# Performance work log

Hardware: AMD Instinct MI355X
Metric: run time of the kernel (lower is better)

Reference implementation:

```python
import jax, jax.numpy as jnp
import numpy as np

H = 512


def setup_inputs() -> dict:
    key = jax.random.key(0)
    ks = jax.random.split(key, 20)
    B, S, T, V, WD = 128, 80, 28, 8000, 1024
    sc = 0.02
    return {
        "encoder_hidden_state": jax.random.normal(ks[0], (1, B, H), jnp.float32),
        "encoder_outputs": jax.random.normal(ks[1], (B, S, H), jnp.float32),
        "target_sentences": jax.random.randint(ks[2], (B, T), 0, V),
        "training_steps": -200,
        "emb": jax.random.normal(ks[3], (V, WD), jnp.float32) * sc,
        "fc1_w": jax.random.normal(ks[4], (H, 2 * H), jnp.float32) * sc,
        "fc1_b": jnp.zeros((H,), jnp.float32),
        "fc2_w": jax.random.normal(ks[5], (H, H), jnp.float32) * sc,
        "fc2_b": jnp.zeros((H,), jnp.float32),
        "fc3_w": jax.random.normal(ks[6], (H, H), jnp.float32) * sc,
        "fc3_b": jnp.zeros((H,), jnp.float32),
        "fc4_w": jax.random.normal(ks[7], (H, H), jnp.float32) * sc,
        "fc4_b": jnp.zeros((H,), jnp.float32),
        "attn_w": jax.random.normal(ks[8], (H,), jnp.float32) * sc,
        "w_ih": jax.random.normal(ks[9], (4 * H, H + WD), jnp.float32) * sc,
        "w_hh": jax.random.normal(ks[10], (4 * H, H), jnp.float32) * sc,
        "b_ih": jnp.zeros((4 * H,), jnp.float32),
        "b_hh": jnp.zeros((4 * H,), jnp.float32),
        "out_w": jax.random.normal(ks[11], (V, H), jnp.float32) * sc,
        "out_b": jnp.zeros((V,), jnp.float32),
    }


def reference(encoder_hidden_state, encoder_outputs, target_sentences, training_steps,
              emb, fc1_w, fc1_b, fc2_w, fc2_b, fc3_w, fc3_b, fc4_w, fc4_b,
              attn_w, w_ih, w_hh, b_ih, b_hh, out_w, out_b):
    # With training_steps=-200, teacher-forcing threshold expit(-9.15)~1e-4, so
    # random.uniform(0.05,0.995) > threshold always holds -> target embedding used every step.
    tgt_emb = emb[target_sentences]              # (B, T, WD)
    xs = jnp.swapaxes(tgt_emb[:, :-1], 0, 1)     # (T-1, B, WD)
    h0 = encoder_hidden_state[0]                 # (B, H)
    c0 = jnp.zeros_like(h0)

    def step(carry, x_t):
        h, c = carry
        # additive-style attention: 4 stacked Linear layers (no nonlinearity, as in source)
        hs = jnp.broadcast_to(h[:, None, :], encoder_outputs.shape)
        z = jnp.concatenate([encoder_outputs, hs], axis=-1)      # (B, S, 2H)
        a = z @ fc1_w.T + fc1_b
        a = a @ fc2_w.T + fc2_b
        a = a @ fc3_w.T + fc3_b
        a = a @ fc4_w.T + fc4_b
        scores = a @ attn_w                                       # (B, S)
        wts = jax.nn.softmax(scores, axis=1)
        ctx = jnp.einsum('bs,bsd->bd', wts, encoder_outputs)      # (B, H)
        # single LSTM step (torch gate order i, f, g, o)
        li = jnp.concatenate([x_t, ctx], axis=1)                  # (B, WD+H)
        gates = li @ w_ih.T + b_ih + h @ w_hh.T + b_hh
        i_, f_, g_, o_ = jnp.split(gates, 4, axis=1)
        c_new = jax.nn.sigmoid(f_) * c + jax.nn.sigmoid(i_) * jnp.tanh(g_)
        h_new = jax.nn.sigmoid(o_) * jnp.tanh(c_new)
        logits = h_new @ out_w.T + out_b                          # (B, V)
        return (h_new, c_new), logits

    _, logits = jax.lax.scan(step, (h0, c0), xs)                  # (T-1, B, V)
    logits = jnp.swapaxes(logits, 0, 1)                           # (B, T-1, V)
    preds = jnp.argmax(logits, axis=2)
    return logits, preds
```

## Files before the change

kernel.cpp:

```cpp
#include <hip/hip_runtime.h>
#include <math.h>

#define BB 128
#define SS 80
#define HH 512
#define TT 27
#define TFULL 28
#define VV 8000

typedef __attribute__((ext_vector_type(4))) float f32x4;
typedef __attribute__((ext_vector_type(8))) short bfrag;

#define OFF_VA   0
#define OFF_VB   512
#define OFF_U    1024
#define OFF_PART 1536
#define OFF_CTX  17920
#define OFF_GB   83456
#define OFF_XG   345600
#define OFF_BAR  7423488
#define FP32_WS_FLOATS 7489536
#define O_H3     0
#define O_WHI    3670016
#define O_WLO    4718592
#define O_R      5767168
#define O_A3X    O_R
#define O_B3X    (O_R + 10616832)
#define O_B3L    O_R

__device__ __forceinline__ unsigned short f2bf(float x) {
    unsigned int u = __float_as_uint(x);
    unsigned int r = (u + 0x7fff + ((u >> 16) & 1)) >> 16;
    return (unsigned short)r;
}
__device__ __forceinline__ float bf2f(unsigned short h) {
    return __uint_as_float(((unsigned int)h) << 16);
}
__device__ __forceinline__ void gload16(void* lds, const void* g) {
    __builtin_amdgcn_global_load_lds(
        (__attribute__((address_space(1))) void*)g,
        (__attribute__((address_space(3))) void*)lds, 16, 0, 0);
}
__device__ __forceinline__ void gload16s(void* lds, const void* g) {
    __builtin_amdgcn_global_load_lds(
        (__attribute__((address_space(1))) void*)g,
        (__attribute__((address_space(3))) void*)lds, 16, 0, 1);
}

__global__ __launch_bounds__(256) void zero_bar(unsigned* b) {
    int i = blockIdx.x * 256 + threadIdx.x;
    if (i < 16512) b[i] = 0u;
}

__global__ __launch_bounds__(256) void conv_split(
    const float* __restrict__ src, int ld, int koff, int K,
    int mode, int bside, const int* __restrict__ gidx,
    unsigned short* __restrict__ dst)
{
    int r = blockIdx.x;
    int sr = r;
    if (mode == 1) { int b = r & 127, t = r >> 7; sr = gidx[b * TFULL + t]; }
    const float* s = src + (size_t)sr * ld + koff;
    unsigned short* d = dst + (size_t)r * (3 * K);
    int off_mid = bside ? 2 * K : K;
    int off_lo  = bside ? K : 2 * K;
    for (int c = threadIdx.x * 4; c < K; c += 1024) {
        float4 v = *(const float4*)(s + c);
        ushort4 hi, lo;
        hi.x = f2bf(v.x); lo.x = f2bf(v.x - bf2f(hi.x));
        hi.y = f2bf(v.y); lo.y = f2bf(v.y - bf2f(hi.y));
        hi.z = f2bf(v.z); lo.z = f2bf(v.z - bf2f(hi.z));
        hi.w = f2bf(v.w); lo.w = f2bf(v.w - bf2f(hi.w));
        *(ushort4*)(d + c) = hi;
        *(ushort4*)(d + off_mid + c) = hi;
        *(ushort4*)(d + off_lo + c) = lo;
    }
}

__global__ __launch_bounds__(256) void conv_splitc(
    const float* __restrict__ src, unsigned short* __restrict__ dst)
{
    int r = blockIdx.x;
    const float* s = src + (size_t)r * 512;
    unsigned short* d = dst + (size_t)r * 1024;
    int c = threadIdx.x * 2;
    float2 v = *(const float2*)(s + c);
    unsigned short hx = f2bf(v.x), hy = f2bf(v.y);
    d[c] = hx; d[c + 1] = hy;
    d[512 + c] = f2bf(v.x - bf2f(hx));
    d[512 + c + 1] = f2bf(v.y - bf2f(hy));
}

__global__ __launch_bounds__(256) void conv_splitw(
    const float* __restrict__ src,
    unsigned short* __restrict__ whi, unsigned short* __restrict__ wlo)
{
    int r = blockIdx.x;
    int sr = (r & 3) * 512 + (r >> 2);
    const float* s = src + (size_t)sr * 512;
    int c = threadIdx.x * 2;
    float2 v = *(const float2*)(s + c);
    unsigned short hx = f2bf(v.x), hy = f2bf(v.y);
    whi[(size_t)r * 512 + c] = hx;
    whi[(size_t)r * 512 + c + 1] = hy;
    wlo[(size_t)r * 512 + c] = f2bf(v.x - bf2f(hx));
    wlo[(size_t)r * 512 + c + 1] = f2bf(v.y - bf2f(hy));
}

__global__ __launch_bounds__(256) void gemm_bf16_nt(
    int M, int N, int K3,
    const unsigned short* __restrict__ A3, int astride, int ahalf,
    const unsigned short* __restrict__ B3,
    const float* __restrict__ bias,
    const float* __restrict__ addmat,
    float* __restrict__ C, int outMode)
{
    __shared__ unsigned short Asm[128 * 64];
    __shared__ unsigned short Bsm[128 * 64];
    int tid = threadIdx.x, wave = tid >> 6, lane = tid & 63;

    int nT = gridDim.x, mT = gridDim.y;
    int p = blockIdx.y * nT + blockIdx.x;
    int nwg = nT * mT;
    int q = nwg >> 3, rr = nwg & 7;
    int xcd = p & 7, pos = p >> 3;
    int lid = (xcd < rr) ? (xcd * (q + 1) + pos) : (rr * (q + 1) + (xcd - rr) * q + pos);
    const int GROUP = 9;
    int width = GROUP * nT;
    int gid2 = lid / width;
    int first_m = gid2 * GROUP;
    int gsz = mT - first_m; if (gsz > GROUP) gsz = GROUP;
    int rem = lid - gid2 * width;
    int mt = first_m + rem % gsz;
    int nt = rem / gsz;
    int m0 = mt * 128, n0 = nt * 128;

    int wm0 = (wave >> 1) * 64, wn0 = (wave & 1) * 64;
    f32x4 acc[4][4];
    #pragma unroll
    for (int i = 0; i < 4; ++i)
        #pragma unroll
        for (int j = 0; j < 4; ++j) acc[i][j] = (f32x4){0.f, 0.f, 0.f, 0.f};

    int srow8 = lane >> 3;
    int schunk = lane & 7;
    for (int k0 = 0; k0 < K3; k0 += 64) {
        int ek0 = ahalf ? (k0 >= 512 ? k0 - 512 : k0) : k0;
        #pragma unroll
        for (int rep = 0; rep < 4; ++rep) {
            int ci = wave * 4 + rep;
            int row = ci * 8 + srow8;
            int sc = schunk ^ (row & 7);
            int gm = m0 + row; if (gm >= M) gm = M - 1;
            gload16(Asm + ci * 512 + lane * 8,
                    A3 + (size_t)gm * astride + ek0 + sc * 8);
            int gn = n0 + row; if (gn >= N) gn = N - 1;
            gload16(Bsm + ci * 512 + lane * 8,
                    B3 + (size_t)gn * K3 + k0 + sc * 8);
        }
        __syncthreads();
        #pragma unroll
        for (int ks = 0; ks < 2; ++ks) {
            bfrag a[4], b[4];
            #pragma unroll
            for (int i = 0; i < 4; ++i) {
                int ar = wm0 + i * 16 + (lane & 15);
                int ab = (ar * 128 + ks * 64 + (lane >> 4) * 16) ^ ((ar & 7) << 4);
                a[i] = *(const bfrag*)((const char*)Asm + ab);
                int br = wn0 + i * 16 + (lane & 15);
                int bb = (br * 128 + ks * 64 + (lane >> 4) * 16) ^ ((br & 7) << 4);
                b[i] = *(const bfrag*)((const char*)Bsm + bb);
            }
            #pragma unroll
            for (int i = 0; i < 4; ++i)
                #pragma unroll
                for (int j = 0; j < 4; ++j)
                    acc[i][j] = __builtin_amdgcn_mfma_f32_16x16x32_bf16(a[i], b[j], acc[i][j], 0, 0, 0);
        }
        __syncthreads();
    }
    #pragma unroll
    for (int i = 0; i < 4; ++i) {
        #pragma unroll
        for (int r = 0; r < 4; ++r) {
            int m = m0 + wm0 + i * 16 + ((lane >> 4) << 2) + r;
            if (m >= M) continue;
            #pragma unroll
            for (int j = 0; j < 4; ++j) {
                int n = n0 + wn0 + j * 16 + (lane & 15);
                if (n >= N) continue;
                float v = acc[i][j][r];
                if (bias) v += bias[n];
                if (addmat) v += addmat[(size_t)(m & 127) * 2048 + n];
                size_t oi;
                if (outMode == 0) oi = (size_t)m * N + n;
                else { int bb2 = m & 127, tt = m >> 7; oi = ((size_t)bb2 * TT + tt) * (size_t)VV + n; }
                C[oi] = v;
            }
        }
    }
}

__global__ __launch_bounds__(256, 1) void lstm_persist4(
    unsigned short* __restrict__ H3,
    const unsigned short* __restrict__ Whi,
    const unsigned short* __restrict__ Wlo,
    const float* __restrict__ xgb,
    unsigned* bar)
{
    __shared__ unsigned short Wl[64 * 512];
    __shared__ unsigned short Al[16 * 1024];
    __shared__ int s_ids[2];

    int tid = threadIdx.x, wv = tid >> 6, lane = tid & 63;
    if (tid == 0) {
        unsigned x;
        asm volatile("s_getreg_b32 %0, hwreg(HW_REG_XCC_ID)" : "=s"(x));
        x &= 7u;
        unsigned s = __hip_atomic_fetch_add(bar + 16384 + x * 16, 1u,
                        __ATOMIC_RELAXED, __HIP_MEMORY_SCOPE_AGENT);
        s_ids[0] = (int)x;
        s_ids[1] = (int)(s & 31u);
    }
    __syncthreads();
    int xcd = s_ids[0], slot = s_ids[1];
    int b0 = xcd * 16;
    int nq0 = slot * 64;

    int l15 = lane & 15, g4 = (lane >> 4) << 4;
    int arow = l15;
    int wr = wv * 16 + l15;
    int n_local = wv * 16 + l15;
    int g = n_local & 3;
    int kglob = slot * 16 + (n_local >> 2);
    const unsigned short* wloRow = Wlo + (size_t)(nq0 + n_local) * 512;
    float creg[4] = {0.f, 0.f, 0.f, 0.f};

    {
        const unsigned short* Wsrc = Whi + (size_t)nq0 * 512;
        #pragma unroll
        for (int j = 0; j < 16; ++j) {
            int ci = j * 256 + tid;
            int row = ci >> 6, cc = ci & 63;
            int sc = cc ^ (row & 7);
            gload16(Wl + ci * 8, Wsrc + (size_t)row * 512 + sc * 8);
        }
        asm volatile("s_waitcnt vmcnt(0)" ::: "memory");
    }
    __syncthreads();

    for (int t = 0; t < TT; ++t) {
        const unsigned short* Asrc = H3 + ((size_t)t * 128 + b0) * 1024;
        #pragma unroll
        for (int j = 0; j < 8; ++j) {
            int ci = j * 256 + tid;
            int row = ci >> 7, cc = ci & 127;
            int sc = cc ^ (row & 7);
            gload16s(Al + ci * 8, Asrc + (size_t)row * 1024 + sc * 8);
        }
        asm volatile("s_waitcnt vmcnt(0)" ::: "memory");
        __syncthreads();

        f32x4 acc0 = (f32x4){0.f, 0.f, 0.f, 0.f};
        f32x4 acc1 = acc0;
        #pragma unroll
        for (int c = 0; c < 16; ++c) {
            int ab = (arow * 2048 + c * 64 + g4) ^ ((arow & 7) << 4);
            int wb = (wr * 1024 + c * 64 + g4) ^ ((wr & 7) << 4);
            bfrag a = *(const bfrag*)((const char*)Al + ab);
            bfrag w = *(const bfrag*)((const char*)Wl + wb);
            if (c & 1) acc1 = __builtin_amdgcn_mfma_f32_16x16x32_bf16(a, w, acc1, 0, 0, 0);
            else       acc0 = __builtin_amdgcn_mfma_f32_16x16x32_bf16(a, w, acc0, 0, 0, 0);
        }
        #pragma unroll
        for (int c = 0; c < 16; ++c) {
            int ab = (arow * 2048 + c * 64 + g4) ^ ((arow & 7) << 4);
            bfrag a = *(const bfrag*)((const char*)Al + ab);
            bfrag w = *(const bfrag*)(wloRow + c * 32 + (lane >> 4) * 8);
            if (c & 1) acc1 = __builtin_amdgcn_mfma_f32_16x16x32_bf16(a, w, acc1, 0, 0, 0);
            else       acc0 = __builtin_amdgcn_mfma_f32_16x16x32_bf16(a, w, acc0, 0, 0, 0);
        }
        #pragma unroll
        for (int c = 0; c < 16; ++c) {
            int ab = (arow * 2048 + (16 + c) * 64 + g4) ^ ((arow & 7) << 4);
            int wb = (wr * 1024 + c * 64 + g4) ^ ((wr & 7) << 4);
            bfrag a = *(const bfrag*)((const char*)Al + ab);
            bfrag w = *(const bfrag*)((const char*)Wl + wb);
            if (c & 1) acc1 = __builtin_amdgcn_mfma_f32_16x16x32_bf16(a, w, acc1, 0, 0, 0);
            else       acc0 = __builtin_amdgcn_mfma_f32_16x16x32_bf16(a, w, acc0, 0, 0, 0);
        }
        f32x4 accT = acc0 + acc1;

        #pragma unroll
        for (int r = 0; r < 4; ++r) {
            int m_local = ((lane >> 4) << 2) + r;
            int b = b0 + m_local;
            float v = accT[r] +
                      xgb[(((size_t)t * 128 + b) << 11) + (size_t)g * 512 + kglob];
            float f1 = __shfl_down(v, 1);
            float f2 = __shfl_down(v, 2);
            float f3 = __shfl_down(v, 3);
            if ((lane & 3) == 0) {
                float si = 1.f / (1.f + expf(-v));
                float sf = 1.f / (1.f + expf(-f1));
                float tg = tanhf(f2);
                float so = 1.f / (1.f + expf(-f3));
                float cn = sf * creg[r] + si * tg;
                float hn = so * tanhf(cn);
                creg[r] = cn;
                unsigned short hi = f2bf(hn);
                unsigned short lo = f2bf(hn - bf2f(hi));
                unsigned short* hr = H3 + ((size_t)(t + 1) * 128 + b) * 1024;
                hr[kglob] = hi; hr[512 + kglob] = lo;
            }
        }

        if (t != TT - 1) {
            asm volatile("s_waitcnt vmcnt(0)" ::: "memory");
            __syncthreads();
            unsigned ph = (unsigned)(t + 1);
            if (tid == 0)
                __hip_atomic_store(bar + xcd * 2048 + slot * 16, ph,
                                   __ATOMIC_RELAXED, __HIP_MEMORY_SCOPE_AGENT);
            if (tid < 32) {
                unsigned* fl = bar + xcd * 2048 + tid * 16;
                while (__hip_atomic_load(fl, __ATOMIC_RELAXED,
                                         __HIP_MEMORY_SCOPE_AGENT) < ph)
                    __builtin_amdgcn_s_sleep(1);
            }
            __syncthreads();
        }
    }
}

__global__ __launch_bounds__(512) void matvec_col_partial(
    const float* __restrict__ W, int ldw, int koff,
    const float* __restrict__ vin, float* __restrict__ part)
{
    int k = threadIdx.x;
    int o0 = blockIdx.x * 16;
    float acc = 0.f;
    #pragma unroll
    for (int o = 0; o < 16; ++o)
        acc += W[(size_t)(o0 + o) * ldw + koff + k] * vin[o0 + o];
    part[blockIdx.x * 512 + k] = acc;
}

__global__ __launch_bounds__(512) void matvec_combine(
    const float* __restrict__ part, float* __restrict__ vout)
{
    int k = threadIdx.x;
    float s = 0.f;
    #pragma unroll
    for (int c = 0; c < 32; ++c) s += part[c * 512 + k];
    vout[k] = s;
}

__global__ __launch_bounds__(256) void attn_ctx(
    const float* __restrict__ enc, const float* __restrict__ u,
    float* __restrict__ ctx)
{
    __shared__ float su[HH];
    __shared__ float sw[SS];
    __shared__ float ssum;
    int b = blockIdx.x, tid = threadIdx.x;
    su[tid] = u[tid];
    su[tid + 256] = u[tid + 256];
    __syncthreads();
    const float* eb = enc + (size_t)b * SS * HH;
    int wave = tid >> 6, lane = tid & 63;
    for (int s = wave; s < SS; s += 4) {
        const float* row = eb + s * HH;
        float acc = 0.f;
        for (int k = lane; k < HH; k += 64) acc += row[k] * su[k];
        #pragma unroll
        for (int off = 32; off; off >>= 1) acc += __shfl_down(acc, off);
        if (lane == 0) sw[s] = acc;
    }
    __syncthreads();
    if (tid == 0) {
        float mx = sw[0];
        for (int s = 1; s < SS; ++s) mx = fmaxf(mx, sw[s]);
        float sum = 0.f;
        for (int s = 0; s < SS; ++s) { float e = expf(sw[s] - mx); sw[s] = e; sum += e; }
        ssum = sum;
    }
    __syncthreads();
    float inv = 1.0f / ssum;
    for (int k = tid; k < HH; k += 256) {
        float acc = 0.f;
        #pragma unroll 4
        for (int s = 0; s < SS; ++s) acc += sw[s] * eb[s * HH + k];
        ctx[(size_t)b * HH + k] = acc * inv;
    }
}

__global__ __launch_bounds__(256) void gemm_nt(
    int M, int N, int K,
    const float* __restrict__ A, int lda,
    const float* __restrict__ Bm, int ldb, int kob,
    const float* __restrict__ bias1, const float* __restrict__ bias2,
    float* __restrict__ C)
{
    __shared__ float As[16][132];
    __shared__ float Bs[16][132];
    int tid = threadIdx.x;
    int m0 = blockIdx.y * 128, n0 = blockIdx.x * 128;
    int tn = tid & 15, tm = tid >> 4;
    float acc[8][8];
    #pragma unroll
    for (int i = 0; i < 8; ++i)
        #pragma unroll
        for (int j = 0; j < 8; ++j) acc[i][j] = 0.f;
    int lr = tid >> 2;
    int lk = (tid & 3) * 4;
    for (int k0 = 0; k0 < K; k0 += 16) {
        #pragma unroll
        for (int half = 0; half < 2; ++half) {
            int mr = lr + half * 64;
            int m = m0 + mr;
            float4 va = make_float4(0.f, 0.f, 0.f, 0.f);
            if (m < M) va = *(const float4*)(A + (size_t)m * lda + k0 + lk);
            As[lk + 0][mr] = va.x; As[lk + 1][mr] = va.y;
            As[lk + 2][mr] = va.z; As[lk + 3][mr] = va.w;
            int n = n0 + mr;
            float4 vb = make_float4(0.f, 0.f, 0.f, 0.f);
            if (n < N) vb = *(const float4*)(Bm + (size_t)n * ldb + kob + k0 + lk);
            Bs[lk + 0][mr] = vb.x; Bs[lk + 1][mr] = vb.y;
            Bs[lk + 2][mr] = vb.z; Bs[lk + 3][mr] = vb.w;
        }
        __syncthreads();
        #pragma unroll
        for (int kk = 0; kk < 16; ++kk) {
            float4 a0 = *(const float4*)&As[kk][tm * 8];
            float4 a1 = *(const float4*)&As[kk][tm * 8 + 4];
            float4 b0 = *(const float4*)&Bs[kk][tn * 8];
            float4 b1 = *(const float4*)&Bs[kk][tn * 8 + 4];
            float av[8] = {a0.x, a0.y, a0.z, a0.w, a1.x, a1.y, a1.z, a1.w};
            float bv[8] = {b0.x, b0.y, b0.z, b0.w, b1.x, b1.y, b1.z, b1.w};
            #pragma unroll
            for (int i = 0; i < 8; ++i)
                #pragma unroll
                for (int j = 0; j < 8; ++j)
                    acc[i][j] += av[i] * bv[j];
        }
        __syncthreads();
    }
    #pragma unroll
    for (int i = 0; i < 8; ++i) {
        int m = m0 + tm * 8 + i;
        if (m >= M) continue;
        #pragma unroll
        for (int j = 0; j < 8; ++j) {
            int n = n0 + tn * 8 + j;
            if (n >= N) continue;
            float v = acc[i][j];
            if (bias1) v += bias1[n];
            if (bias2) v += bias2[n];
            C[(size_t)m * N + n] = v;
        }
    }
}

__global__ __launch_bounds__(256) void argmax_k(
    const float* __restrict__ logits, float* __restrict__ preds)
{
    int r = blockIdx.x * 4 + (threadIdx.x >> 6);
    int lane = threadIdx.x & 63;
    const float* row = logits + (size_t)r * VV;
    float best = -INFINITY;
    int bi = 0;
    for (int v = lane; v < VV; v += 64) {
        float x = row[v];
        if (x > best) { best = x; bi = v; }
    }
    #pragma unroll
    for (int off = 32; off; off >>= 1) {
        float ob = __shfl_down(best, off);
        int oi = __shfl_down(bi, off);
        if (ob > best || (ob == best && oi < bi)) { best = ob; bi = oi; }
    }
    if (lane == 0) preds[r] = (float)bi;
}

extern "C" void kernel_launch(void* const* d_in, const int* in_sizes, int n_in,
                              void* d_out, int out_size, void* d_ws, size_t ws_size,
                              hipStream_t stream) {
    const float* ehs   = (const float*)d_in[0];
    const float* enc   = (const float*)d_in[1];
    const int*   tgt   = (const int*)d_in[2];
    const float* emb   = (const float*)d_in[4];
    const float* fc1w  = (const float*)d_in[5];
    const float* fc2w  = (const float*)d_in[7];
    const float* fc3w  = (const float*)d_in[9];
    const float* fc4w  = (const float*)d_in[11];
    const float* attnw = (const float*)d_in[13];
    const float* wih   = (const float*)d_in[14];
    const float* whh   = (const float*)d_in[15];
    const float* bih   = (const float*)d_in[16];
    const float* bhh   = (const float*)d_in[17];
    const float* outw  = (const float*)d_in[18];
    const float* outb  = (const float*)d_in[19];
    float* out = (float*)d_out;
    float* ws  = (float*)d_ws;

    float* vA   = ws + OFF_VA;
    float* vB   = ws + OFF_VB;
    float* u    = ws + OFF_U;
    float* part = ws + OFF_PART;
    float* ctx  = ws + OFF_CTX;
    float* gb   = ws + OFF_GB;
    float* xg   = ws + OFF_XG;
    unsigned* bar = (unsigned*)(ws + OFF_BAR);
    unsigned short* bfb = (unsigned short*)(ws + FP32_WS_FLOATS);
    unsigned short* H3   = bfb + O_H3;
    unsigned short* WHI  = bfb + O_WHI;
    unsigned short* WLO  = bfb + O_WLO;
    unsigned short* A3X  = bfb + O_A3X;
    unsigned short* B3X  = bfb + O_B3X;
    unsigned short* B3L  = bfb + O_B3L;

    matvec_col_partial<<<32, 512, 0, stream>>>(fc4w, 512, 0, attnw, part);
    matvec_combine<<<1, 512, 0, stream>>>(part, vA);
    matvec_col_partial<<<32, 512, 0, stream>>>(fc3w, 512, 0, vA, part);
    matvec_combine<<<1, 512, 0, stream>>>(part, vB);
    matvec_col_partial<<<32, 512, 0, stream>>>(fc2w, 512, 0, vB, part);
    matvec_combine<<<1, 512, 0, stream>>>(part, vA);
    matvec_col_partial<<<32, 512, 0, stream>>>(fc1w, 1024, 0, vA, part);
    matvec_combine<<<1, 512, 0, stream>>>(part, u);

    attn_ctx<<<128, 256, 0, stream>>>(enc, u, ctx);

    {
        dim3 g(16, 1);
        gemm_nt<<<g, 256, 0, stream>>>(128, 2048, 512, ctx, 512,
                                       wih, 1536, 1024, bih, bhh, gb);
    }

    conv_split<<<2048, 256, 0, stream>>>(wih, 1536, 0, 1024, 0, 1, nullptr, B3X);
    conv_split<<<3456, 256, 0, stream>>>(emb, 1024, 0, 1024, 1, 0, tgt, A3X);
    {
        dim3 g(16, 27);
        gemm_bf16_nt<<<g, 256, 0, stream>>>(3456, 2048, 3072, A3X, 3072, 0, B3X,
                                            nullptr, gb, xg, 0);
    }

    conv_split<<<8000, 256, 0, stream>>>(outw, 512, 0, 512, 0, 1, nullptr, B3L);
    conv_splitw<<<2048, 256, 0, stream>>>(whh, WHI, WLO);
    conv_splitc<<<128, 256, 0, stream>>>(ehs, H3);

    zero_bar<<<65, 256, 0, stream>>>(bar);
    lstm_persist4<<<256, 256, 0, stream>>>(H3, WHI, WLO, xg, bar);

    {
        dim3 g(63, 27);
        gemm_bf16_nt<<<g, 256, 0, stream>>>(3456, 8000, 1536,
                                            H3 + (size_t)128 * 1024, 1024, 1, B3L,
                                            outb, nullptr, out, 1);
    }

    argmax_k<<<864, 256, 0, stream>>>(out, out + (size_t)TT * 128 * VV);
}
```

Measured before the change: 653.7 us.

## Double-buffer GEMM LDS tiles, prefetch LSTM input gates, use nontemporal output stores

The bf16 GEMM now uses two LDS buffers, issuing loads for tile k+2 while computing tile k and waiting with partial vmcnt, so global-load latency overlaps the MFMA work. The GEMM output stores become nontemporal to avoid cache pollution from the large logits write. In the persistent LSTM kernel, the xgb input-gate values are loaded before the MFMA loop alongside the H tile loads instead of after it. Doubling LDS per block may reduce occupancy, and the vmcnt counts must match the number of issued loads exactly.

```diff
diff --git a/kernel.cpp b/kernel.cpp
--- a/kernel.cpp
+++ b/kernel.cpp
@@ -115,8 +115,8 @@
     const float* __restrict__ addmat,
     float* __restrict__ C, int outMode)
 {
-    __shared__ unsigned short Asm[128 * 64];
-    __shared__ unsigned short Bsm[128 * 64];
+    __shared__ unsigned short Asm[2][128 * 64];
+    __shared__ unsigned short Bsm[2][128 * 64];
     int tid = threadIdx.x, wave = tid >> 6, lane = tid & 63;
 
     int nT = gridDim.x, mT = gridDim.y;
@@ -144,7 +144,8 @@
 
     int srow8 = lane >> 3;
     int schunk = lane & 7;
-    for (int k0 = 0; k0 < K3; k0 += 64) {
+
+    auto STAGE = [&](int buf, int k0) {
         int ek0 = ahalf ? (k0 >= 512 ? k0 - 512 : k0) : k0;
         #pragma unroll
         for (int rep = 0; rep < 4; ++rep) {
@@ -152,13 +153,23 @@
             int row = ci * 8 + srow8;
             int sc = schunk ^ (row & 7);
             int gm = m0 + row; if (gm >= M) gm = M - 1;
-            gload16(Asm + ci * 512 + lane * 8,
+            gload16(Asm[buf] + ci * 512 + lane * 8,
                     A3 + (size_t)gm * astride + ek0 + sc * 8);
             int gn = n0 + row; if (gn >= N) gn = N - 1;
-            gload16(Bsm + ci * 512 + lane * 8,
+            gload16(Bsm[buf] + ci * 512 + lane * 8,
                     B3 + (size_t)gn * K3 + k0 + sc * 8);
         }
-        __syncthreads();
+    };
+
+    int nK = K3 >> 6;
+    STAGE(0, 0);
+    STAGE(1, 64);
+    for (int kc = 0; kc < nK; ++kc) {
+        if (kc < nK - 1) asm volatile("s_waitcnt vmcnt(8)" ::: "memory");
+        else             asm volatile("s_waitcnt vmcnt(0)" ::: "memory");
+        __builtin_amdgcn_s_barrier();
+        const unsigned short* Ab = Asm[kc & 1];
+        const unsigned short* Bb = Bsm[kc & 1];
         #pragma unroll
         for (int ks = 0; ks < 2; ++ks) {
             bfrag a[4], b[4];
@@ -166,10 +177,10 @@
             for (int i = 0; i < 4; ++i) {
                 int ar = wm0 + i * 16 + (lane & 15);
                 int ab = (ar * 128 + ks * 64 + (lane >> 4) * 16) ^ ((ar & 7) << 4);
-                a[i] = *(const bfrag*)((const char*)Asm + ab);
+                a[i] = *(const bfrag*)((const char*)Ab + ab);
                 int br = wn0 + i * 16 + (lane & 15);
                 int bb = (br * 128 + ks * 64 + (lane >> 4) * 16) ^ ((br & 7) << 4);
-                b[i] = *(const bfrag*)((const char*)Bsm + bb);
+                b[i] = *(const bfrag*)((const char*)Bb + bb);
             }
             #pragma unroll
             for (int i = 0; i < 4; ++i)
@@ -177,7 +188,8 @@
                 for (int j = 0; j < 4; ++j)
                     acc[i][j] = __builtin_amdgcn_mfma_f32_16x16x32_bf16(a[i], b[j], acc[i][j], 0, 0, 0);
         }
-        __syncthreads();
+        __builtin_amdgcn_s_barrier();
+        if (kc + 2 < nK) STAGE(kc & 1, (kc + 2) * 64);
     }
     #pragma unroll
     for (int i = 0; i < 4; ++i) {
@@ -195,7 +207,7 @@
                 size_t oi;
                 if (outMode == 0) oi = (size_t)m * N + n;
                 else { int bb2 = m & 127, tt = m >> 7; oi = ((size_t)bb2 * TT + tt) * (size_t)VV + n; }
-                C[oi] = v;
+                __builtin_nontemporal_store(v, &C[oi]);
             }
         }
     }
@@ -258,8 +270,14 @@
             int sc = cc ^ (row & 7);
             gload16s(Al + ci * 8, Asrc + (size_t)row * 1024 + sc * 8);
         }
-        asm volatile("s_waitcnt vmcnt(0)" ::: "memory");
-        __syncthreads();
+        float xpre[4];
+        #pragma unroll
+        for (int r = 0; r < 4; ++r) {
+            int m_local = ((lane >> 4) << 2) + r;
+            xpre[r] = xgb[(((size_t)t * 128 + b0 + m_local) << 11) + (size_t)g * 512 + kglob];
+        }
+        asm volatile("s_waitcnt vmcnt(4)" ::: "memory");
+        __builtin_amdgcn_s_barrier();
 
         f32x4 acc0 = (f32x4){0.f, 0.f, 0.f, 0.f};
         f32x4 acc1 = acc0;
@@ -295,8 +313,7 @@
         for (int r = 0; r < 4; ++r) {
             int m_local = ((lane >> 4) << 2) + r;
             int b = b0 + m_local;
-            float v = accT[r] +
-                      xgb[(((size_t)t * 128 + b) << 11) + (size_t)g * 512 + kglob];
+            float v = accT[r] + xpre[r];
             float f1 = __shfl_down(v, 1);
             float f2 = __shfl_down(v, 2);
             float f3 = __shfl_down(v, 3);
```

After: 623.3 us. 1.05x faster.
